# Kernel tuning notes

Measured on AMD Instinct MI355X. Metric: run time of the kernel, lower is better.

Reference implementation:

```python
import jax, jax.numpy as jnp
import numpy as np

N, E = 50000, 800000
NDIM_IN, EDIM, HID, NDIM_OUT, NCLS = 64, 64, 128, 128, 10


def _linear_params(k, fan_in, fan_out):
    lim = 1.0 / np.sqrt(fan_in)
    kw, kb = jax.random.split(k)
    W = jax.random.uniform(kw, (fan_in, fan_out), minval=-lim, maxval=lim, dtype=jnp.float32)
    b = jax.random.uniform(kb, (fan_out,), minval=-lim, maxval=lim, dtype=jnp.float32)
    return W, b


def setup_inputs() -> dict:
    key = jax.random.key(0)
    ks = jax.random.split(key, 9)
    Wm1, bm1 = _linear_params(ks[0], NDIM_IN + EDIM, HID)      # layer1 W_msg
    Wa1, ba1 = _linear_params(ks[1], NDIM_IN + HID, HID)       # layer1 W_apply
    Wm2, bm2 = _linear_params(ks[2], HID + EDIM, NDIM_OUT)     # layer2 W_msg
    Wa2, ba2 = _linear_params(ks[3], HID + NDIM_OUT, NDIM_OUT) # layer2 W_apply
    Wp, bp = _linear_params(ks[4], 2 * NDIM_OUT, NCLS)         # edge predictor
    nfeats = jax.random.normal(ks[5], (N, NDIM_IN), dtype=jnp.float32)
    efeats = jax.random.normal(ks[6], (E, EDIM), dtype=jnp.float32)
    src = jax.random.randint(ks[7], (E,), 0, N)
    dst = jax.random.randint(ks[8], (E,), 0, N)
    return dict(nfeats=nfeats, efeats=efeats, src=src, dst=dst,
                Wm1=Wm1, bm1=bm1, Wa1=Wa1, ba1=ba1,
                Wm2=Wm2, bm2=bm2, Wa2=Wa2, ba2=ba2, Wp=Wp, bp=bp)


def _sage_layer(h, efeats, src, dst, Wm, bm, Wa, ba):
    # per-edge message: W_msg([h_src || e])
    m = jnp.concatenate([h[src], efeats], axis=1) @ Wm + bm          # [E, out]
    # mean aggregation by destination node (0 for zero in-degree, as in DGL fn.mean)
    s = jax.ops.segment_sum(m, dst, num_segments=N)                  # [N, out]
    deg = jax.ops.segment_sum(jnp.ones((E,), m.dtype), dst, num_segments=N)
    h_neigh = s / jnp.maximum(deg, 1.0)[:, None]
    return jax.nn.relu(jnp.concatenate([h, h_neigh], axis=1) @ Wa + ba)


def reference(nfeats, efeats, src, dst, Wm1, bm1, Wa1, ba1, Wm2, bm2, Wa2, ba2, Wp, bp):
    h = _sage_layer(nfeats, efeats, src, dst, Wm1, bm1, Wa1, ba1)
    # dropout between layers is identity in eval mode
    h = _sage_layer(h, efeats, src, dst, Wm2, bm2, Wa2, ba2)
    # MLPPredictor: per-edge score = W([h_u || h_v])
    score = jnp.concatenate([h[src], h[dst]], axis=1) @ Wp + bp      # [E, 10]
    return score
```

## Files before the change

kernel.cpp:

```cpp
#include <hip/hip_runtime.h>

typedef float  f32x4 __attribute__((ext_vector_type(4)));
typedef short  s16x8 __attribute__((ext_vector_type(8)));
typedef unsigned int u32x4 __attribute__((ext_vector_type(4)));

#define DEVINL __device__ __forceinline__

DEVINL float4 ld4(const float* p) { return *reinterpret_cast<const float4*>(p); }
DEVINL f32x4 ld4v(const float* p) { return *reinterpret_cast<const f32x4*>(p); }
DEVINL u32x4 ld4u(const unsigned* p) { return *reinterpret_cast<const u32x4*>(p); }
DEVINL f32x4 ld4nt(const float* p) {
  return __builtin_nontemporal_load(reinterpret_cast<const f32x4*>(p));
}

DEVINL unsigned pack1(float f) {
  unsigned u = __float_as_uint(f);
  unsigned hb = (u + 0x7fffu + ((u >> 16) & 1u)) & 0xffff0000u;
  float l = f - __uint_as_float(hb);
  unsigned v = __float_as_uint(l);
  unsigned lb = (v + 0x7fffu + ((v >> 16) & 1u)) >> 16;
  return hb | lb;
}
DEVINL float unpack1(unsigned v) {
  return __uint_as_float(v & 0xffff0000u) + __uint_as_float(v << 16);
}
DEVINL f32x4 unpack4(u32x4 v) {
  f32x4 r;
  #pragma unroll
  for (int i = 0; i < 4; ++i) r[i] = unpack1(v[i]);
  return r;
}
DEVINL void unpack_frag(u32x4 a, u32x4 b, s16x8& ah, s16x8& al) {
  u32x4 H, L;
  H[0] = (a[0] >> 16) | (a[1] & 0xffff0000u);
  H[1] = (a[2] >> 16) | (a[3] & 0xffff0000u);
  H[2] = (b[0] >> 16) | (b[1] & 0xffff0000u);
  H[3] = (b[2] >> 16) | (b[3] & 0xffff0000u);
  L[0] = (a[0] & 0xffffu) | (a[1] << 16);
  L[1] = (a[2] & 0xffffu) | (a[3] << 16);
  L[2] = (b[0] & 0xffffu) | (b[1] << 16);
  L[3] = (b[2] & 0xffffu) | (b[3] << 16);
  ah = __builtin_bit_cast(s16x8, H);
  al = __builtin_bit_cast(s16x8, L);
}

DEVINL void split1(float f, unsigned short& h, unsigned short& l) {
  unsigned u = __float_as_uint(f);
  unsigned hb = (u + 0x7fffu + ((u >> 16) & 1u)) >> 16;
  float hf = __uint_as_float(hb << 16);
  float d = f - hf;
  unsigned v = __float_as_uint(d);
  unsigned lb = (v + 0x7fffu + ((v >> 16) & 1u)) >> 16;
  h = (unsigned short)hb;
  l = (unsigned short)lb;
}

__global__ __launch_bounds__(256) void prep_kernel(
    const float* __restrict__ Wm1, const float* __restrict__ Wa1, const float* __restrict__ bm1,
    const float* __restrict__ Wm2, const float* __restrict__ Wa2, const float* __restrict__ bm2,
    float* __restrict__ bmw1, float* __restrict__ bmw2,
    unsigned short* __restrict__ w1h, unsigned short* __restrict__ w1l,
    unsigned short* __restrict__ w2h, unsigned short* __restrict__ w2l,
    const float* __restrict__ nf, unsigned* __restrict__ nfp, int nelem,
    const int* __restrict__ dst, int* __restrict__ deg, int E, int npack)
{
  int blk = blockIdx.x;
  if (blk < 257) {
    int b = blk * 2 + (threadIdx.x >> 7);
    int j = threadIdx.x & 127;
    unsigned short h, l;
    if (b < 128) {
      float acc = 0.f;
      for (int k = 0; k < 128; ++k) acc = fmaf(Wm1[b * 128 + k], Wa1[(64 + k) * 128 + j], acc);
      split1(acc, h, l);
      w1h[(size_t)j * 192 + 64 + b] = h;
      w1l[(size_t)j * 192 + 64 + b] = l;
    } else if (b < 320) {
      int i = b - 128;
      float acc = 0.f;
      for (int k = 0; k < 128; ++k) acc = fmaf(Wm2[i * 128 + k], Wa2[(128 + k) * 128 + j], acc);
      split1(acc, h, l);
      w2h[(size_t)j * 320 + 128 + i] = h;
      w2l[(size_t)j * 320 + 128 + i] = l;
    } else if (b == 320) {
      float acc = 0.f;
      for (int k = 0; k < 128; ++k) acc = fmaf(bm1[k], Wa1[(64 + k) * 128 + j], acc);
      bmw1[j] = acc;
    } else if (b == 321) {
      float acc = 0.f;
      for (int k = 0; k < 128; ++k) acc = fmaf(bm2[k], Wa2[(128 + k) * 128 + j], acc);
      bmw2[j] = acc;
    } else if (b < 386) {
      int t = b - 322;
      split1(Wa1[t * 128 + j], h, l);
      w1h[(size_t)j * 192 + t] = h;
      w1l[(size_t)j * 192 + t] = l;
    } else {
      int t = b - 386;
      split1(Wa2[t * 128 + j], h, l);
      w2h[(size_t)j * 320 + t] = h;
      w2l[(size_t)j * 320 + t] = l;
    }
  } else if (blk < 257 + npack) {
    int idx = (blk - 257) * 256 + threadIdx.x;
    if (idx < nelem) nfp[idx] = pack1(nf[idx]);
  } else {
    int e = (blk - 257 - npack) * 256 + threadIdx.x;
    if (e < E) atomicAdd(&deg[dst[e]], 1);
  }
}

__global__ __launch_bounds__(256) void scan_blk_kernel(
    const int* __restrict__ in, int* __restrict__ excl, int* __restrict__ bsum, int n)
{
  __shared__ int tmp[256];
  int t = threadIdx.x;
  int i = blockIdx.x * 256 + t;
  int v = (i < n) ? in[i] : 0;
  tmp[t] = v;
  __syncthreads();
  #pragma unroll
  for (int off = 1; off < 256; off <<= 1) {
    int add = (t >= off) ? tmp[t - off] : 0;
    __syncthreads();
    tmp[t] += add;
    __syncthreads();
  }
  if (i < n) excl[i] = tmp[t] - v;
  if (t == 255) bsum[blockIdx.x] = tmp[255];
}

__global__ __launch_bounds__(256) void finalize2_kernel(
    const int* __restrict__ excl, const int* __restrict__ bsum, int nblk,
    int* __restrict__ rp, int* __restrict__ cursor, int N, int E)
{
  __shared__ int bs[256];
  int t = threadIdx.x;
  bs[t] = (t < nblk) ? bsum[t] : 0;
  __syncthreads();
  #pragma unroll
  for (int off = 1; off < 256; off <<= 1) {
    int add = (t >= off) ? bs[t - off] : 0;
    __syncthreads();
    bs[t] += add;
    __syncthreads();
  }
  int i = blockIdx.x * 256 + t;
  if (i < N) {
    int blk = i >> 8;
    int boff = blk ? bs[blk - 1] : 0;
    int v = excl[i] + boff;
    rp[i] = v;
    cursor[i] = v;
  }
  if (i == N) rp[N] = E;
}

__global__ __launch_bounds__(256) void scatter_kernel(
    const int* __restrict__ dst, const int* __restrict__ src,
    int* __restrict__ cursor, int2* __restrict__ es, int E)
{
  int e = blockIdx.x * 256 + threadIdx.x;
  if (e >= E) return;
  int d = dst[e];
  int pos = atomicAdd(&cursor[d], 1);
  es[pos] = make_int2(e, src[e]);
}

__global__ __launch_bounds__(256) void csr_agg_l1_kernel(
    const float* __restrict__ ef, const float* __restrict__ nf,
    const int2* __restrict__ es, const int* __restrict__ rp,
    unsigned* __restrict__ mEp, unsigned* __restrict__ mH1p, int N)
{
  int node = (int)((blockIdx.x * 256u + threadIdx.x) >> 6);
  node = __builtin_amdgcn_readfirstlane(node);
  if (node >= N) return;
  const int lane = threadIdx.x & 63;
  const int g = lane >> 4, l16 = lane & 15;
  const int beg = rp[node], end = rp[node + 1];
  const int full_end = beg + ((end - beg) & ~15);

  f32x4 ea = {0.f, 0.f, 0.f, 0.f}, ha = {0.f, 0.f, 0.f, 0.f};
  int k0 = beg;
  for (; k0 < full_end; k0 += 16) {
    #pragma unroll
    for (int u = 0; u < 4; ++u) {
      int2 p = es[k0 + 4 * u + g];
      ea += ld4nt(ef + (size_t)p.x * 64 + l16 * 4);
      ha += ld4v (nf + (size_t)p.y * 64 + l16 * 4);
    }
  }
  #pragma unroll
  for (int u = 0; u < 4; ++u) {
    int i = k0 + 4 * u + g;
    if (i < end) {
      int2 p = es[i];
      ea += ld4nt(ef + (size_t)p.x * 64 + l16 * 4);
      ha += ld4v (nf + (size_t)p.y * 64 + l16 * 4);
    }
  }
  #pragma unroll
  for (int j = 0; j < 4; ++j) {
    ea[j] += __shfl_xor(ea[j], 16);
    ea[j] += __shfl_xor(ea[j], 32);
    ha[j] += __shfl_xor(ha[j], 16);
    ha[j] += __shfl_xor(ha[j], 32);
  }
  if (g == 0) {
    float inv = 1.0f / fmaxf((float)(end - beg), 1.0f);
    u32x4 pe, ph;
    #pragma unroll
    for (int j = 0; j < 4; ++j) {
      pe[j] = pack1(ea[j] * inv);
      ph[j] = pack1(ha[j] * inv);
    }
    *reinterpret_cast<u32x4*>(mEp  + (size_t)node * 64 + l16 * 4) = pe;
    *reinterpret_cast<u32x4*>(mH1p + (size_t)node * 64 + l16 * 4) = ph;
  }
}

__global__ __launch_bounds__(256) void csr_agg128_kernel(
    const unsigned* __restrict__ X, const int2* __restrict__ es,
    const int* __restrict__ rp, unsigned* __restrict__ out, int N)
{
  int node = (int)((blockIdx.x * 256u + threadIdx.x) >> 6);
  node = __builtin_amdgcn_readfirstlane(node);
  if (node >= N) return;
  const int lane = threadIdx.x & 63;
  const int g = lane >> 5, l32 = lane & 31;
  const int beg = rp[node], end = rp[node + 1];
  const int full_end = beg + ((end - beg) & ~15);

  f32x4 a = {0.f, 0.f, 0.f, 0.f};
  int k0 = beg;
  for (; k0 < full_end; k0 += 16) {
    u32x4 v[8];
    #pragma unroll
    for (int u = 0; u < 8; ++u) {
      int s = es[k0 + 2 * u + g].y;
      v[u] = ld4u(X + (size_t)s * 128 + l32 * 4);
    }
    #pragma unroll
    for (int u = 0; u < 8; ++u) a += unpack4(v[u]);
  }
  #pragma unroll
  for (int u = 0; u < 8; ++u) {
    int i = k0 + 2 * u + g;
    if (i < end) {
      int s = es[i].y;
      a += unpack4(ld4u(X + (size_t)s * 128 + l32 * 4));
    }
  }
  #pragma unroll
  for (int j = 0; j < 4; ++j) a[j] += __shfl_xor(a[j], 32);
  if (g == 0) {
    float inv = 1.0f / fmaxf((float)(end - beg), 1.0f);
    u32x4 pv;
    #pragma unroll
    for (int j = 0; j < 4; ++j) pv[j] = pack1(a[j] * inv);
    *reinterpret_cast<u32x4*>(out + (size_t)node * 128 + l32 * 4) = pv;
  }
}

template<int C1, int C2, int C3>
__global__ __launch_bounds__(256, 2) void fgemm_kernel(
    const unsigned* __restrict__ X1, const unsigned* __restrict__ X2,
    const unsigned* __restrict__ X3,
    const unsigned short* __restrict__ WtHi, const unsigned short* __restrict__ WtLo,
    const float* __restrict__ ba, const float* __restrict__ bmw,
    const int* __restrict__ deg, unsigned* __restrict__ out, int n)
{
  constexpr int K = C1 + C2 + C3;
  const int lane = threadIdx.x & 63;
  const int w = threadIdx.x >> 6;
  const int base = blockIdx.x * 128;
  const int l15 = lane & 15;
  const int lg = lane >> 4;

  f32x4 acc[2][8] = {};

  #pragma unroll
  for (int k0 = 0; k0 < K; k0 += 32) {
    const unsigned* sp;
    int C, off;
    if (k0 < C1)            { sp = X1; C = C1; off = k0; }
    else if (k0 < C1 + C2)  { sp = X2; C = C2; off = k0 - C1; }
    else                    { sp = X3; C = C3; off = k0 - C1 - C2; }
    const int ca = off + lg * 8;

    s16x8 ah[2], al[2];
    #pragma unroll
    for (int mi = 0; mi < 2; ++mi) {
      int row = base + w * 32 + mi * 16 + l15;
      if (row >= n) row = n - 1;
      u32x4 p0 = ld4u(sp + (size_t)row * C + ca);
      u32x4 p1 = ld4u(sp + (size_t)row * C + ca + 4);
      unpack_frag(p0, p1, ah[mi], al[mi]);
    }

    s16x8 bh[8], bl[8];
    const int kb = k0 + lg * 8;
    #pragma unroll
    for (int ni = 0; ni < 8; ++ni) {
      size_t woff = (size_t)(ni * 16 + l15) * K + kb;
      bh[ni] = *reinterpret_cast<const s16x8*>(WtHi + woff);
      bl[ni] = *reinterpret_cast<const s16x8*>(WtLo + woff);
    }

    #pragma unroll
    for (int mi = 0; mi < 2; ++mi)
      #pragma unroll
      for (int ni = 0; ni < 8; ++ni) {
        acc[mi][ni] = __builtin_amdgcn_mfma_f32_16x16x32_bf16(ah[mi], bh[ni], acc[mi][ni], 0, 0, 0);
        acc[mi][ni] = __builtin_amdgcn_mfma_f32_16x16x32_bf16(ah[mi], bl[ni], acc[mi][ni], 0, 0, 0);
        acc[mi][ni] = __builtin_amdgcn_mfma_f32_16x16x32_bf16(al[mi], bh[ni], acc[mi][ni], 0, 0, 0);
      }
  }

  float bav[8], bmv[8];
  #pragma unroll
  for (int ni = 0; ni < 8; ++ni) {
    bav[ni] = ba[ni * 16 + l15];
    bmv[ni] = bmw[ni * 16 + l15];
  }

  #pragma unroll
  for (int mi = 0; mi < 2; ++mi) {
    #pragma unroll
    for (int r = 0; r < 4; ++r) {
      int grow = base + w * 32 + mi * 16 + lg * 4 + r;
      if (grow >= n) continue;
      float msk = deg[grow] > 0 ? 1.0f : 0.0f;
      unsigned* op = out + (size_t)grow * 128 + l15;
      #pragma unroll
      for (int ni = 0; ni < 8; ++ni)
        op[ni * 16] = pack1(fmaxf(acc[mi][ni][r] + bav[ni] + msk * bmv[ni], 0.0f));
    }
  }
}

__global__ __launch_bounds__(256, 2) void fgemm2_pred_kernel(
    const unsigned* __restrict__ X1, const unsigned* __restrict__ X2,
    const unsigned* __restrict__ X3,
    const unsigned short* __restrict__ WtHi, const unsigned short* __restrict__ WtLo,
    const float* __restrict__ ba, const float* __restrict__ bmw,
    const int* __restrict__ deg, const float* __restrict__ Wp,
    const float* __restrict__ bp, float* __restrict__ pt, int n)
{
  constexpr int C1 = 128, C2 = 128, C3 = 64;
  constexpr int K = C1 + C2 + C3;
  __shared__ float xs[128 * 129];
  __shared__ float wl[2560];

  const int tid = threadIdx.x;
  const int lane = tid & 63;
  const int w = tid >> 6;
  const int base = blockIdx.x * 128;
  const int l15 = lane & 15;
  const int lg = lane >> 4;

  for (int i = tid; i < 2560; i += 256) wl[i] = Wp[i];

  f32x4 acc[2][8] = {};

  #pragma unroll
  for (int k0 = 0; k0 < K; k0 += 32) {
    const unsigned* sp;
    int C, off;
    if (k0 < C1)            { sp = X1; C = C1; off = k0; }
    else if (k0 < C1 + C2)  { sp = X2; C = C2; off = k0 - C1; }
    else                    { sp = X3; C = C3; off = k0 - C1 - C2; }
    const int ca = off + lg * 8;

    s16x8 ah[2], al[2];
    #pragma unroll
    for (int mi = 0; mi < 2; ++mi) {
      int row = base + w * 32 + mi * 16 + l15;
      if (row >= n) row = n - 1;
      u32x4 p0 = ld4u(sp + (size_t)row * C + ca);
      u32x4 p1 = ld4u(sp + (size_t)row * C + ca + 4);
      unpack_frag(p0, p1, ah[mi], al[mi]);
    }

    s16x8 bh[8], bl[8];
    const int kb = k0 + lg * 8;
    #pragma unroll
    for (int ni = 0; ni < 8; ++ni) {
      size_t woff = (size_t)(ni * 16 + l15) * K + kb;
      bh[ni] = *reinterpret_cast<const s16x8*>(WtHi + woff);
      bl[ni] = *reinterpret_cast<const s16x8*>(WtLo + woff);
    }

    #pragma unroll
    for (int mi = 0; mi < 2; ++mi)
      #pragma unroll
      for (int ni = 0; ni < 8; ++ni) {
        acc[mi][ni] = __builtin_amdgcn_mfma_f32_16x16x32_bf16(ah[mi], bh[ni], acc[mi][ni], 0, 0, 0);
        acc[mi][ni] = __builtin_amdgcn_mfma_f32_16x16x32_bf16(ah[mi], bl[ni], acc[mi][ni], 0, 0, 0);
        acc[mi][ni] = __builtin_amdgcn_mfma_f32_16x16x32_bf16(al[mi], bh[ni], acc[mi][ni], 0, 0, 0);
      }
  }

  float bav[8], bmv[8];
  #pragma unroll
  for (int ni = 0; ni < 8; ++ni) {
    bav[ni] = ba[ni * 16 + l15];
    bmv[ni] = bmw[ni * 16 + l15];
  }

  #pragma unroll
  for (int mi = 0; mi < 2; ++mi) {
    #pragma unroll
    for (int r = 0; r < 4; ++r) {
      int lr = w * 32 + mi * 16 + lg * 4 + r;
      int grow = base + lr;
      if (grow >= n) continue;
      float msk = deg[grow] > 0 ? 1.0f : 0.0f;
      #pragma unroll
      for (int ni = 0; ni < 8; ++ni)
        xs[lr * 129 + ni * 16 + l15] =
            fmaxf(acc[mi][ni][r] + bav[ni] + msk * bmv[ni], 0.0f);
    }
  }
  __syncthreads();

  const int r = tid >> 1;
  const int half = tid & 1;
  const int grow = base + r;
  if (grow < n) {
    const float* wb = wl + half * 1280;
    float a[10] = {};
    for (int k = 0; k < 128; ++k) {
      float x = xs[r * 129 + k];
      #pragma unroll
      for (int j = 0; j < 10; ++j) a[j] = fmaf(x, wb[k * 10 + j], a[j]);
    }
    float* op = pt + (size_t)grow * 20 + half * 10;
    if (half) {
      #pragma unroll
      for (int j = 0; j < 10; ++j) op[j] = a[j] + bp[j];
    } else {
      #pragma unroll
      for (int j = 0; j < 10; ++j) op[j] = a[j];
    }
  }
}

__global__ __launch_bounds__(256) void pred_edge_kernel(
    const float* __restrict__ pt, const int* __restrict__ src, const int* __restrict__ dst,
    float* __restrict__ out, int E)
{
  int idx = blockIdx.x * 256 + threadIdx.x;
  if (idx >= E * 5) return;
  int e = idx / 5;
  int jj = idx - e * 5;
  int s = src[e], d = dst[e];
  const float2* p2 = (const float2*)pt;
  float2 a = p2[(size_t)s * 10 + jj];
  float2 b = p2[(size_t)d * 10 + 5 + jj];
  ((float2*)out)[idx] = make_float2(a.x + b.x, a.y + b.y);
}

extern "C" void kernel_launch(void* const* d_in, const int* in_sizes, int n_in,
                              void* d_out, int out_size, void* d_ws, size_t ws_size,
                              hipStream_t stream) {
  const float* nfeats = (const float*)d_in[0];
  const float* efeats = (const float*)d_in[1];
  const int*   src    = (const int*)d_in[2];
  const int*   dst    = (const int*)d_in[3];
  const float* Wm1 = (const float*)d_in[4];
  const float* bm1 = (const float*)d_in[5];
  const float* Wa1 = (const float*)d_in[6];
  const float* ba1 = (const float*)d_in[7];
  const float* Wm2 = (const float*)d_in[8];
  const float* bm2 = (const float*)d_in[9];
  const float* Wa2 = (const float*)d_in[10];
  const float* ba2 = (const float*)d_in[11];
  const float* Wp  = (const float*)d_in[12];
  const float* bp  = (const float*)d_in[13];

  const int N = in_sizes[0] / 64;
  const int E = in_sizes[2];
  const int nblk = (N + 255) / 256;

  int* ip     = (int*)d_ws;
  int* deg_i  = ip;
  int* rp     = ip + (size_t)N;
  int* scr    = ip + 2 * (size_t)N + 4 + E;
  int* excl   = scr;
  int* cursor = scr + (size_t)N;
  int* bsum   = scr + 2 * (size_t)N;

  size_t fbase = (4 * (size_t)N + 516 + (size_t)E + 3) & ~(size_t)3;
  float*    fp    = (float*)d_ws;
  unsigned* mEp   = (unsigned*)(fp + fbase);
  float*    pt    = fp + fbase + (size_t)N * 64;
  unsigned* mH1p  = (unsigned*)pt;
  unsigned* mH2p  = (unsigned*)(fp + fbase + (size_t)N * 128);
  unsigned* h1p   = (unsigned*)(fp + fbase + (size_t)N * 384);
  float*    out   = (float*)d_out;

  int2*  es   = (int2*)(fp + fbase + (size_t)N * 512);
  float* wst  = fp + fbase + (size_t)N * 512 + 2 * (size_t)E;
  float* bmw1 = wst;
  float* bmw2 = bmw1 + 128;
  unsigned short* w1h = (unsigned short*)(bmw2 + 128);
  unsigned short* w1l = w1h + 192 * 128;
  unsigned short* w2h = w1l + 192 * 128;
  unsigned short* w2l = w2h + 320 * 128;
  unsigned* nfp = (unsigned*)(w2l + 320 * 128);

  hipMemsetAsync(deg_i, 0, (size_t)N * sizeof(int), stream);

  int gridE  = (E + 255) / 256;
  int gridN  = (N + 127) / 128;
  int gridNW = ((N * 64) + 255) / 256;
  int npack  = (N * 64 + 255) / 256;

  prep_kernel<<<257 + npack + gridE, 256, 0, stream>>>(
      Wm1, Wa1, bm1, Wm2, Wa2, bm2, bmw1, bmw2, w1h, w1l, w2h, w2l,
      nfeats, nfp, N * 64, dst, deg_i, E, npack);

  scan_blk_kernel<<<nblk, 256, 0, stream>>>(deg_i, excl, bsum, N);
  finalize2_kernel<<<(N + 256) / 256, 256, 0, stream>>>(excl, bsum, nblk, rp, cursor, N, E);
  scatter_kernel<<<gridE, 256, 0, stream>>>(dst, src, cursor, es, E);

  csr_agg_l1_kernel<<<gridNW, 256, 0, stream>>>(efeats, nfeats, es, rp, mEp, mH1p, N);
  fgemm_kernel<64, 64, 64><<<gridN, 256, 0, stream>>>(
      nfp, mH1p, mEp, w1h, w1l, ba1, bmw1, deg_i, h1p, N);

  csr_agg128_kernel<<<gridNW, 256, 0, stream>>>(h1p, es, rp, mH2p, N);
  fgemm2_pred_kernel<<<gridN, 256, 0, stream>>>(
      h1p, mH2p, mEp, w2h, w2l, ba2, bmw2, deg_i, Wp, bp, pt, N);

  pred_edge_kernel<<<(E * 5 + 255) / 256, 256, 0, stream>>>(pt, src, dst, out, E);
}
```

Baseline: 345.2 us.

## Split packed hi/lo features into planes and gather only bf16 hi part

Replaces the packed 32-bit hi|lo bf16 representation with separate hi and lo bf16 planes for node features, aggregates and hidden states. The neighbor aggregation kernels now gather only the hi plane, which halves the bytes read per gathered row in both layers. The GEMM kernels load A fragments directly from the two planes and no longer need to unpack them. The cost is that aggregated neighbor features lose the low-order correction bits, so the result is less accurate.

```diff
diff --git a/kernel.cpp b/kernel.cpp
--- a/kernel.cpp
+++ b/kernel.cpp
@@ -2,73 +2,47 @@
 
 typedef float  f32x4 __attribute__((ext_vector_type(4)));
 typedef short  s16x8 __attribute__((ext_vector_type(8)));
-typedef unsigned int u32x4 __attribute__((ext_vector_type(4)));
+typedef unsigned short u16;
+typedef u16    u16x4 __attribute__((ext_vector_type(4)));
 
 #define DEVINL __device__ __forceinline__
 
-DEVINL float4 ld4(const float* p) { return *reinterpret_cast<const float4*>(p); }
-DEVINL f32x4 ld4v(const float* p) { return *reinterpret_cast<const f32x4*>(p); }
-DEVINL u32x4 ld4u(const unsigned* p) { return *reinterpret_cast<const u32x4*>(p); }
 DEVINL f32x4 ld4nt(const float* p) {
   return __builtin_nontemporal_load(reinterpret_cast<const f32x4*>(p));
 }
 
-DEVINL unsigned pack1(float f) {
-  unsigned u = __float_as_uint(f);
-  unsigned hb = (u + 0x7fffu + ((u >> 16) & 1u)) & 0xffff0000u;
-  float l = f - __uint_as_float(hb);
-  unsigned v = __float_as_uint(l);
-  unsigned lb = (v + 0x7fffu + ((v >> 16) & 1u)) >> 16;
-  return hb | lb;
-}
-DEVINL float unpack1(unsigned v) {
-  return __uint_as_float(v & 0xffff0000u) + __uint_as_float(v << 16);
-}
-DEVINL f32x4 unpack4(u32x4 v) {
-  f32x4 r;
-  #pragma unroll
-  for (int i = 0; i < 4; ++i) r[i] = unpack1(v[i]);
-  return r;
-}
-DEVINL void unpack_frag(u32x4 a, u32x4 b, s16x8& ah, s16x8& al) {
-  u32x4 H, L;
-  H[0] = (a[0] >> 16) | (a[1] & 0xffff0000u);
-  H[1] = (a[2] >> 16) | (a[3] & 0xffff0000u);
-  H[2] = (b[0] >> 16) | (b[1] & 0xffff0000u);
-  H[3] = (b[2] >> 16) | (b[3] & 0xffff0000u);
-  L[0] = (a[0] & 0xffffu) | (a[1] << 16);
-  L[1] = (a[2] & 0xffffu) | (a[3] << 16);
-  L[2] = (b[0] & 0xffffu) | (b[1] << 16);
-  L[3] = (b[2] & 0xffffu) | (b[3] << 16);
-  ah = __builtin_bit_cast(s16x8, H);
-  al = __builtin_bit_cast(s16x8, L);
-}
-
-DEVINL void split1(float f, unsigned short& h, unsigned short& l) {
+DEVINL void split1(float f, u16& h, u16& l) {
   unsigned u = __float_as_uint(f);
   unsigned hb = (u + 0x7fffu + ((u >> 16) & 1u)) >> 16;
   float hf = __uint_as_float(hb << 16);
   float d = f - hf;
   unsigned v = __float_as_uint(d);
   unsigned lb = (v + 0x7fffu + ((v >> 16) & 1u)) >> 16;
-  h = (unsigned short)hb;
-  l = (unsigned short)lb;
+  h = (u16)hb;
+  l = (u16)lb;
+}
+
+DEVINL f32x4 bf4_to_f32(u16x4 v) {
+  f32x4 r;
+  #pragma unroll
+  for (int i = 0; i < 4; ++i) r[i] = __uint_as_float(((unsigned)v[i]) << 16);
+  return r;
 }
 
 __global__ __launch_bounds__(256) void prep_kernel(
     const float* __restrict__ Wm1, const float* __restrict__ Wa1, const float* __restrict__ bm1,
     const float* __restrict__ Wm2, const float* __restrict__ Wa2, const float* __restrict__ bm2,
     float* __restrict__ bmw1, float* __restrict__ bmw2,
-    unsigned short* __restrict__ w1h, unsigned short* __restrict__ w1l,
-    unsigned short* __restrict__ w2h, unsigned short* __restrict__ w2l,
-    const float* __restrict__ nf, unsigned* __restrict__ nfp, int nelem,
-    const int* __restrict__ dst, int* __restrict__ deg, int E, int npack)
+    u16* __restrict__ w1h, u16* __restrict__ w1l,
+    u16* __restrict__ w2h, u16* __restrict__ w2l,
+    const float* __restrict__ nf, u16* __restrict__ nfh, u16* __restrict__ nfl,
+    int nelem, const int* __restrict__ dst, int* __restrict__ deg, int E, int npack)
 {
   int blk = blockIdx.x;
   if (blk < 257) {
     int b = blk * 2 + (threadIdx.x >> 7);
     int j = threadIdx.x & 127;
-    unsigned short h, l;
+    u16 h, l;
     if (b < 128) {
       float acc = 0.f;
       for (int k = 0; k < 128; ++k) acc = fmaf(Wm1[b * 128 + k], Wa1[(64 + k) * 128 + j], acc);
@@ -103,7 +77,12 @@
     }
   } else if (blk < 257 + npack) {
     int idx = (blk - 257) * 256 + threadIdx.x;
-    if (idx < nelem) nfp[idx] = pack1(nf[idx]);
+    if (idx < nelem) {
+      u16 h, l;
+      split1(nf[idx], h, l);
+      nfh[idx] = h;
+      nfl[idx] = l;
+    }
   } else {
     int e = (blk - 257 - npack) * 256 + threadIdx.x;
     if (e < E) atomicAdd(&deg[dst[e]], 1);
@@ -168,9 +147,10 @@
 }
 
 __global__ __launch_bounds__(256) void csr_agg_l1_kernel(
-    const float* __restrict__ ef, const float* __restrict__ nf,
+    const float* __restrict__ ef, const u16* __restrict__ nfh,
     const int2* __restrict__ es, const int* __restrict__ rp,
-    unsigned* __restrict__ mEp, unsigned* __restrict__ mH1p, int N)
+    u16* __restrict__ mEh, u16* __restrict__ mEl,
+    u16* __restrict__ mH1h, u16* __restrict__ mH1l, int N)
 {
   int node = (int)((blockIdx.x * 256u + threadIdx.x) >> 6);
   node = __builtin_amdgcn_readfirstlane(node);
@@ -187,7 +167,7 @@
     for (int u = 0; u < 4; ++u) {
       int2 p = es[k0 + 4 * u + g];
       ea += ld4nt(ef + (size_t)p.x * 64 + l16 * 4);
-      ha += ld4v (nf + (size_t)p.y * 64 + l16 * 4);
+      ha += bf4_to_f32(*reinterpret_cast<const u16x4*>(nfh + (size_t)p.y * 64 + l16 * 4));
     }
   }
   #pragma unroll
@@ -196,7 +176,7 @@
     if (i < end) {
       int2 p = es[i];
       ea += ld4nt(ef + (size_t)p.x * 64 + l16 * 4);
-      ha += ld4v (nf + (size_t)p.y * 64 + l16 * 4);
+      ha += bf4_to_f32(*reinterpret_cast<const u16x4*>(nfh + (size_t)p.y * 64 + l16 * 4));
     }
   }
   #pragma unroll
@@ -208,20 +188,24 @@
   }
   if (g == 0) {
     float inv = 1.0f / fmaxf((float)(end - beg), 1.0f);
-    u32x4 pe, ph;
+    u16x4 eh, el, hh, hl;
     #pragma unroll
     for (int j = 0; j < 4; ++j) {
-      pe[j] = pack1(ea[j] * inv);
-      ph[j] = pack1(ha[j] * inv);
-    }
-    *reinterpret_cast<u32x4*>(mEp  + (size_t)node * 64 + l16 * 4) = pe;
-    *reinterpret_cast<u32x4*>(mH1p + (size_t)node * 64 + l16 * 4) = ph;
+      u16 a, b;
+      split1(ea[j] * inv, a, b); eh[j] = a; el[j] = b;
+      split1(ha[j] * inv, a, b); hh[j] = a; hl[j] = b;
+    }
+    size_t o = (size_t)node * 64 + l16 * 4;
+    *reinterpret_cast<u16x4*>(mEh  + o) = eh;
+    *reinterpret_cast<u16x4*>(mEl  + o) = el;
+    *reinterpret_cast<u16x4*>(mH1h + o) = hh;
+    *reinterpret_cast<u16x4*>(mH1l + o) = hl;
   }
 }
 
 __global__ __launch_bounds__(256) void csr_agg128_kernel(
-    const unsigned* __restrict__ X, const int2* __restrict__ es,
-    const int* __restrict__ rp, unsigned* __restrict__ out, int N)
+    const u16* __restrict__ h1h, const int2* __restrict__ es,
+    const int* __restrict__ rp, u16* __restrict__ mH2h, u16* __restrict__ mH2l, int N)
 {
   int node = (int)((blockIdx.x * 256u + threadIdx.x) >> 6);
   node = __builtin_amdgcn_readfirstlane(node);
@@ -234,41 +218,48 @@
   f32x4 a = {0.f, 0.f, 0.f, 0.f};
   int k0 = beg;
   for (; k0 < full_end; k0 += 16) {
-    u32x4 v[8];
+    u16x4 v[8];
     #pragma unroll
     for (int u = 0; u < 8; ++u) {
       int s = es[k0 + 2 * u + g].y;
-      v[u] = ld4u(X + (size_t)s * 128 + l32 * 4);
-    }
-    #pragma unroll
-    for (int u = 0; u < 8; ++u) a += unpack4(v[u]);
+      v[u] = *reinterpret_cast<const u16x4*>(h1h + (size_t)s * 128 + l32 * 4);
+    }
+    #pragma unroll
+    for (int u = 0; u < 8; ++u) a += bf4_to_f32(v[u]);
   }
   #pragma unroll
   for (int u = 0; u < 8; ++u) {
     int i = k0 + 2 * u + g;
     if (i < end) {
       int s = es[i].y;
-      a += unpack4(ld4u(X + (size_t)s * 128 + l32 * 4));
+      a += bf4_to_f32(*reinterpret_cast<const u16x4*>(h1h + (size_t)s * 128 + l32 * 4));
     }
   }
   #pragma unroll
   for (int j = 0; j < 4; ++j) a[j] += __shfl_xor(a[j], 32);
   if (g == 0) {
     float inv = 1.0f / fmaxf((float)(end - beg), 1.0f);
-    u32x4 pv;
-    #pragma unroll
-    for (int j = 0; j < 4; ++j) pv[j] = pack1(a[j] * inv);
-    *reinterpret_cast<u32x4*>(out + (size_t)node * 128 + l32 * 4) = pv;
+    u16x4 ph, pl;
+    #pragma unroll
+    for (int j = 0; j < 4; ++j) {
+      u16 x, y;
+      split1(a[j] * inv, x, y);
+      ph[j] = x; pl[j] = y;
+    }
+    size_t o = (size_t)node * 128 + l32 * 4;
+    *reinterpret_cast<u16x4*>(mH2h + o) = ph;
+    *reinterpret_cast<u16x4*>(mH2l + o) = pl;
   }
 }
 
 template<int C1, int C2, int C3>
 __global__ __launch_bounds__(256, 2) void fgemm_kernel(
-    const unsigned* __restrict__ X1, const unsigned* __restrict__ X2,
-    const unsigned* __restrict__ X3,
-    const unsigned short* __restrict__ WtHi, const unsigned short* __restrict__ WtLo,
+    const u16* __restrict__ X1h, const u16* __restrict__ X1l,
+    const u16* __restrict__ X2h, const u16* __restrict__ X2l,
+    const u16* __restrict__ X3h, const u16* __restrict__ X3l,
+    const u16* __restrict__ WtHi, const u16* __restrict__ WtLo,
     const float* __restrict__ ba, const float* __restrict__ bmw,
-    const int* __restrict__ deg, unsigned* __restrict__ out, int n)
+    const int* __restrict__ deg, u16* __restrict__ outH, u16* __restrict__ outL, int n)
 {
   constexpr int K = C1 + C2 + C3;
   const int lane = threadIdx.x & 63;
@@ -281,11 +272,11 @@
 
   #pragma unroll
   for (int k0 = 0; k0 < K; k0 += 32) {
-    const unsigned* sp;
+    const u16 *sph, *spl;
     int C, off;
-    if (k0 < C1)            { sp = X1; C = C1; off = k0; }
-    else if (k0 < C1 + C2)  { sp = X2; C = C2; off = k0 - C1; }
-    else                    { sp = X3; C = C3; off = k0 - C1 - C2; }
+    if (k0 < C1)            { sph = X1h; spl = X1l; C = C1; off = k0; }
+    else if (k0 < C1 + C2)  { sph = X2h; spl = X2l; C = C2; off = k0 - C1; }
+    else                    { sph = X3h; spl = X3l; C = C3; off = k0 - C1 - C2; }
     const int ca = off + lg * 8;
 
     s16x8 ah[2], al[2];
@@ -293,9 +284,8 @@
     for (int mi = 0; mi < 2; ++mi) {
       int row = base + w * 32 + mi * 16 + l15;
       if (row >= n) row = n - 1;
-      u32x4 p0 = ld4u(sp + (size_t)row * C + ca);
-      u32x4 p1 = ld4u(sp + (size_t)row * C + ca + 4);
-      unpack_frag(p0, p1, ah[mi], al[mi]);
+      ah[mi] = *reinterpret_cast<const s16x8*>(sph + (size_t)row * C + ca);
+      al[mi] = *reinterpret_cast<const s16x8*>(spl + (size_t)row * C + ca);
     }
 
     s16x8 bh[8], bl[8];
@@ -331,18 +321,25 @@
       int grow = base + w * 32 + mi * 16 + lg * 4 + r;
       if (grow >= n) continue;
       float msk = deg[grow] > 0 ? 1.0f : 0.0f;
-      unsigned* op = out + (size_t)grow * 128 + l15;
-      #pragma unroll
-      for (int ni = 0; ni < 8; ++ni)
-        op[ni * 16] = pack1(fmaxf(acc[mi][ni][r] + bav[ni] + msk * bmv[ni], 0.0f));
+      u16* oph = outH + (size_t)grow * 128 + l15;
+      u16* opl = outL + (size_t)grow * 128 + l15;
+      #pragma unroll
+      for (int ni = 0; ni < 8; ++ni) {
+        float v = fmaxf(acc[mi][ni][r] + bav[ni] + msk * bmv[ni], 0.0f);
+        u16 h, l;
+        split1(v, h, l);
+        oph[ni * 16] = h;
+        opl[ni * 16] = l;
+      }
     }
   }
 }
 
 __global__ __launch_bounds__(256, 2) void fgemm2_pred_kernel(
-    const unsigned* __restrict__ X1, const unsigned* __restrict__ X2,
-    const unsigned* __restrict__ X3,
-    const unsigned short* __restrict__ WtHi, const unsigned short* __restrict__ WtLo,
+    const u16* __restrict__ X1h, const u16* __restrict__ X1l,
+    const u16* __restrict__ X2h, const u16* __restrict__ X2l,
+    const u16* __restrict__ X3h, const u16* __restrict__ X3l,
+    const u16* __restrict__ WtHi, const u16* __restrict__ WtLo,
     const float* __restrict__ ba, const float* __restrict__ bmw,
     const int* __restrict__ deg, const float* __restrict__ Wp,
     const float* __restrict__ bp, float* __restrict__ pt, int n)
@@ -365,11 +362,11 @@
 
   #pragma unroll
   for (int k0 = 0; k0 < K; k0 += 32) {
-    const unsigned* sp;
+    const u16 *sph, *spl;
     int C, off;
-    if (k0 < C1)            { sp = X1; C = C1; off = k0; }
-    else if (k0 < C1 + C2)  { sp = X2; C = C2; off = k0 - C1; }
-    else                    { sp = X3; C = C3; off = k0 - C1 - C2; }
+    if (k0 < C1)            { sph = X1h; spl = X1l; C = C1; off = k0; }
+    else if (k0 < C1 + C2)  { sph = X2h; spl = X2l; C = C2; off = k0 - C1; }
+    else                    { sph = X3h; spl = X3l; C = C3; off = k0 - C1 - C2; }
     const int ca = off + lg * 8;
 
     s16x8 ah[2], al[2];
@@ -377,9 +374,8 @@
     for (int mi = 0; mi < 2; ++mi) {
       int row = base + w * 32 + mi * 16 + l15;
       if (row >= n) row = n - 1;
-      u32x4 p0 = ld4u(sp + (size_t)row * C + ca);
-      u32x4 p1 = ld4u(sp + (size_t)row * C + ca + 4);
-      unpack_frag(p0, p1, ah[mi], al[mi]);
+      ah[mi] = *reinterpret_cast<const s16x8*>(sph + (size_t)row * C + ca);
+      al[mi] = *reinterpret_cast<const s16x8*>(spl + (size_t)row * C + ca);
     }
 
     s16x8 bh[8], bl[8];
@@ -492,23 +488,28 @@
   int* bsum   = scr + 2 * (size_t)N;
 
   size_t fbase = (4 * (size_t)N + 516 + (size_t)E + 3) & ~(size_t)3;
-  float*    fp    = (float*)d_ws;
-  unsigned* mEp   = (unsigned*)(fp + fbase);
-  float*    pt    = fp + fbase + (size_t)N * 64;
-  unsigned* mH1p  = (unsigned*)pt;
-  unsigned* mH2p  = (unsigned*)(fp + fbase + (size_t)N * 128);
-  unsigned* h1p   = (unsigned*)(fp + fbase + (size_t)N * 384);
-  float*    out   = (float*)d_out;
+  float* fp   = (float*)d_ws;
+  u16* mEh  = (u16*)(fp + fbase);
+  u16* mEl  = mEh + (size_t)N * 64;
+  float* pt = fp + fbase + (size_t)N * 64;
+  u16* mH1h = (u16*)pt;
+  u16* mH1l = mH1h + (size_t)N * 64;
+  u16* mH2h = (u16*)(fp + fbase + (size_t)N * 128);
+  u16* mH2l = mH2h + (size_t)N * 128;
+  u16* h1h  = (u16*)(fp + fbase + (size_t)N * 384);
+  u16* h1l  = h1h + (size_t)N * 128;
+  float* out = (float*)d_out;
 
   int2*  es   = (int2*)(fp + fbase + (size_t)N * 512);
   float* wst  = fp + fbase + (size_t)N * 512 + 2 * (size_t)E;
   float* bmw1 = wst;
   float* bmw2 = bmw1 + 128;
-  unsigned short* w1h = (unsigned short*)(bmw2 + 128);
-  unsigned short* w1l = w1h + 192 * 128;
-  unsigned short* w2h = w1l + 192 * 128;
-  unsigned short* w2l = w2h + 320 * 128;
-  unsigned* nfp = (unsigned*)(w2l + 320 * 128);
+  u16* w1h = (u16*)(bmw2 + 128);
+  u16* w1l = w1h + 192 * 128;
+  u16* w2h = w1l + 192 * 128;
+  u16* w2l = w2h + 320 * 128;
+  u16* nfh = w2l + 320 * 128;
+  u16* nfl = nfh + (size_t)N * 64;
 
   hipMemsetAsync(deg_i, 0, (size_t)N * sizeof(int), stream);
 
@@ -519,19 +520,20 @@
 
   prep_kernel<<<257 + npack + gridE, 256, 0, stream>>>(
       Wm1, Wa1, bm1, Wm2, Wa2, bm2, bmw1, bmw2, w1h, w1l, w2h, w2l,
-      nfeats, nfp, N * 64, dst, deg_i, E, npack);
+      nfeats, nfh, nfl, N * 64, dst, deg_i, E, npack);
 
   scan_blk_kernel<<<nblk, 256, 0, stream>>>(deg_i, excl, bsum, N);
   finalize2_kernel<<<(N + 256) / 256, 256, 0, stream>>>(excl, bsum, nblk, rp, cursor, N, E);
   scatter_kernel<<<gridE, 256, 0, stream>>>(dst, src, cursor, es, E);
 
-  csr_agg_l1_kernel<<<gridNW, 256, 0, stream>>>(efeats, nfeats, es, rp, mEp, mH1p, N);
+  csr_agg_l1_kernel<<<gridNW, 256, 0, stream>>>(
+      efeats, nfh, es, rp, mEh, mEl, mH1h, mH1l, N);
   fgemm_kernel<64, 64, 64><<<gridN, 256, 0, stream>>>(
-      nfp, mH1p, mEp, w1h, w1l, ba1, bmw1, deg_i, h1p, N);
-
-  csr_agg128_kernel<<<gridNW, 256, 0, stream>>>(h1p, es, rp, mH2p, N);
+      nfh, nfl, mH1h, mH1l, mEh, mEl, w1h, w1l, ba1, bmw1, deg_i, h1h, h1l, N);
+
+  csr_agg128_kernel<<<gridNW, 256, 0, stream>>>(h1h, es, rp, mH2h, mH2l, N);
   fgemm2_pred_kernel<<<gridN, 256, 0, stream>>>(
-      h1p, mH2p, mEp, w2h, w2l, ba2, bmw2, deg_i, Wp, bp, pt, N);
+      h1h, h1l, mH2h, mH2l, mEh, mEl, w2h, w2l, ba2, bmw2, deg_i, Wp, bp, pt, N);
 
   pred_edge_kernel<<<(E * 5 + 255) / 256, 256, 0, stream>>>(pt, src, dst, out, E);
 }
```

Measured after the change: 315.8 us. 1.09x faster.
